# Performance work log

Hardware: AMD Instinct MI355X
Metric: run time of the kernel (lower is better)

Reference implementation:

```python
import jax, jax.numpy as jnp
import numpy as np

B, D, K, H, N = 2048, 3, 64, 768, 4096  # batch, tree depth, fanout, hidden, internal nodes


def setup_inputs() -> dict:
    key = jax.random.key(0)
    k1, k2, k3, k4, k5 = jax.random.split(key, 5)
    pooled = jax.random.normal(k1, (B, H), dtype=jnp.float32)
    nodes = jax.random.randint(k2, (B, D), 0, N)            # per-sample fc head ids along the label path
    path = jax.random.randint(k3, (B, D), 0, K)             # per-node CE target (child index)
    W = jax.random.normal(k4, (N, K, H), dtype=jnp.float32) * 0.02  # stacked nn.Linear weights
    b = jax.random.normal(k5, (N, K), dtype=jnp.float32) * 0.02     # stacked nn.Linear biases
    return {"pooled": pooled, "nodes": nodes, "path": path, "W": W, "b": b}


def reference(pooled, nodes, path, W, b):
    # Gather each sample's tiny linear heads along its label path: [B, D, K, H]
    Wg = W[nodes]
    bg = b[nodes]                                            # [B, D, K]
    # Per-sample, per-depth gemv: fc[n](feature) for n in nodes
    logits = jnp.einsum('bdkh,bh->bdk', Wg, pooled) + bg     # [B, D, K]
    # Per-node CrossEntropyLoss against path targets, summed over the path
    lse = jax.nn.logsumexp(logits, axis=-1)                  # [B, D]
    tgt = jnp.take_along_axis(logits, path[..., None], axis=-1)[..., 0]  # [B, D]
    losses = jnp.sum(lse - tgt, axis=-1)                     # [B]
    return losses, logits
```

## Files before the change

### kernel.cpp

```cpp
#include <hip/hip_runtime.h>
#include <hip/hip_bf16.h>

#define BATCH   2048
#define DEPTH   3
#define FANOUT  64
#define HID     768
#define NNODES  4096
#define NPAIRS  (BATCH * DEPTH)
#define CAP     16
#define NTAIL   64
#define SCHUNK  4

#define WS_COUNT 0
#define WS_OCNT  NNODES
#define WS_LIST  (NNODES + 4)
#define WS_OVFL  (WS_LIST + NNODES * CAP)
#define WS_ZERO_INTS (NNODES + 4)

__global__ __launch_bounds__(256) void bin_kernel(const int* __restrict__ nodes,
                                                  int* __restrict__ ws) {
    int idx = blockIdx.x * 256 + threadIdx.x;
    if (idx >= NPAIRS) return;
    int n = nodes[idx];
    int pos = atomicAdd(&ws[WS_COUNT + n], 1);
    if (pos < CAP) {
        ws[WS_LIST + n * CAP + pos] = idx;
    } else {
        int op = atomicAdd(&ws[WS_OCNT], 1);
        ws[WS_OVFL + op] = idx;
    }
}

template <int SC>
__device__ __forceinline__ void compute_rows(
    const float4* __restrict__ w4,
    const float (*s_pool)[HID],
    float (*s_log)[FANOUT],
    const float* s_bias,
    int wave, int lane)
{
#pragma unroll 4
    for (int kk = 0; kk < 16; ++kk) {
        const int k = wave * 16 + kk;
        const float4* wr = w4 + (size_t)k * (HID / 4);
        float4 w0 = wr[lane], w1 = wr[lane + 64], w2 = wr[lane + 128];
        float v[SC];
#pragma unroll
        for (int s = 0; s < SC; ++s) {
            const float4* a4 = reinterpret_cast<const float4*>(&s_pool[s][0]);
            float4 a0 = a4[lane], a1 = a4[lane + 64], a2 = a4[lane + 128];
            v[s] = w0.x * a0.x + w0.y * a0.y + w0.z * a0.z + w0.w * a0.w
                 + w1.x * a1.x + w1.y * a1.y + w1.z * a1.z + w1.w * a1.w
                 + w2.x * a2.x + w2.y * a2.y + w2.z * a2.z + w2.w * a2.w;
        }
#pragma unroll
        for (int off = 32; off > 0; off >>= 1) {
#pragma unroll
            for (int s = 0; s < SC; ++s)
                v[s] += __shfl_xor(v[s], off, 64);
        }
        if (lane == 0) {
#pragma unroll
            for (int s = 0; s < SC; ++s)
                s_log[s][k] = v[s] + s_bias[k];
        }
    }
}

__global__ __launch_bounds__(256) void node_gemm_kernel(
    const float* __restrict__ pooled,
    const float* __restrict__ W,
    const float* __restrict__ bias,
    const int*   __restrict__ nodes,
    int*         __restrict__ ws,
    float*       __restrict__ logits)
{
    __shared__ int   s_pairs[CAP];
    __shared__ float s_bias[FANOUT];
    __shared__ float s_pool[SCHUNK][HID];
    __shared__ float s_log[SCHUNK][FANOUT];

    const int tid  = threadIdx.x;
    const int wave = tid >> 6;
    const int lane = tid & 63;

    int c = 0;
    int n = -1;

    if (blockIdx.x < NNODES) {
        n = blockIdx.x;
        c = ws[WS_COUNT + n];
        if (c == 0) return;
        c = min(c, CAP);
        if (tid < c) s_pairs[tid] = ws[WS_LIST + (size_t)n * CAP + tid];
    } else {
        const int oc = min(ws[WS_OCNT], NPAIRS);
        const int i  = (int)blockIdx.x - NNODES;
        if (i >= oc) return;
        c = 1;
        if (tid == 0) s_pairs[0] = ws[WS_OVFL + i];
        __syncthreads();
        n = nodes[s_pairs[0]];
    }
    if (tid < FANOUT) s_bias[tid] = bias[(size_t)n * FANOUT + tid];
    __syncthreads();

    const float4* w4 = reinterpret_cast<const float4*>(W + (size_t)n * FANOUT * HID);

    for (int base = 0; base < c; base += SCHUNK) {
        const int sc = min(c - base, SCHUNK);
        const int* pair_chunk = s_pairs + base;

        for (int idx = tid; idx < sc * (HID / 4); idx += 256) {
            int s = idx / (HID / 4);
            int f = idx % (HID / 4);
            int b = pair_chunk[s] / DEPTH;
            reinterpret_cast<float4*>(&s_pool[s][0])[f] =
                reinterpret_cast<const float4*>(pooled + (size_t)b * HID)[f];
        }
        __syncthreads();

        switch (sc) {
        case 1: compute_rows<1>(w4, s_pool, s_log, s_bias, wave, lane); break;
        case 2: compute_rows<2>(w4, s_pool, s_log, s_bias, wave, lane); break;
        case 3: compute_rows<3>(w4, s_pool, s_log, s_bias, wave, lane); break;
        default: compute_rows<4>(w4, s_pool, s_log, s_bias, wave, lane); break;
        }
        __syncthreads();

        for (int idx = tid; idx < sc * FANOUT; idx += 256) {
            int s = idx >> 6, k = idx & 63;
            logits[(size_t)pair_chunk[s] * FANOUT + k] = s_log[s][k];
        }
        __syncthreads();
    }
}

__global__ __launch_bounds__(256) void loss_kernel(
    const float* __restrict__ logits,
    const int*   __restrict__ path,
    float*       __restrict__ losses)
{
    const int wave = threadIdx.x >> 6;
    const int lane = threadIdx.x & 63;
    const int b = blockIdx.x * 4 + wave;
    if (b >= BATCH) return;
    const float* lg = logits + (size_t)b * DEPTH * FANOUT;
    float loss = 0.f;
#pragma unroll
    for (int d = 0; d < DEPTH; ++d) {
        float x = lg[d * FANOUT + lane];
        float m = x;
#pragma unroll
        for (int off = 32; off > 0; off >>= 1)
            m = fmaxf(m, __shfl_xor(m, off, 64));
        float e = expf(x - m);
#pragma unroll
        for (int off = 32; off > 0; off >>= 1)
            e += __shfl_xor(e, off, 64);
        float lse = m + logf(e);
        int t = path[b * DEPTH + d];
        loss += lse - __shfl(x, t, 64);
    }
    if (lane == 0) losses[b] = loss;
}

extern "C" void kernel_launch(void* const* d_in, const int* in_sizes, int n_in,
                              void* d_out, int out_size, void* d_ws, size_t ws_size,
                              hipStream_t stream) {
    const float* pooled = (const float*)d_in[0];
    const int*   nodes  = (const int*)d_in[1];
    const int*   path   = (const int*)d_in[2];
    const float* W      = (const float*)d_in[3];
    const float* bias   = (const float*)d_in[4];

    float* losses = (float*)d_out;
    float* logits = (float*)d_out + BATCH;
    int*   ws     = (int*)d_ws;

    hipMemsetAsync(ws, 0, WS_ZERO_INTS * sizeof(int), stream);
    hipLaunchKernelGGL(bin_kernel, dim3((NPAIRS + 255) / 256), dim3(256),
                       0, stream, nodes, ws);
    hipLaunchKernelGGL(node_gemm_kernel, dim3(NNODES + NTAIL), dim3(256),
                       0, stream, pooled, W, bias, nodes, ws, logits);
    hipLaunchKernelGGL(loss_kernel, dim3((BATCH + 3) / 4), dim3(256),
                       0, stream, logits, path, losses);
}
```

Measured before the change: 134.9 us.

## Fuse binning, node GEMV and loss into one persistent cooperative kernel

Replaces the three launches (binning, per-node GEMV, loss) with a single cooperative persistent kernel. Blocks pull work from an atomic queue that holds only the active nodes, and each node's per-pair cross-entropy term is computed in place while the logits are still in shared memory. Grid-wide syncs separate the phases, and a final pass sums the per-depth terms. This removes launch gaps and idle blocks for unused nodes, at the cost of grid.sync overhead, contention on the atomic queue, and a fallback path if the cooperative launch fails.

```diff
diff --git a/kernel.cpp b/kernel.cpp
--- a/kernel.cpp
+++ b/kernel.cpp
@@ -1,5 +1,8 @@
 #include <hip/hip_runtime.h>
 #include <hip/hip_bf16.h>
+#include <hip/hip_cooperative_groups.h>
+
+namespace cg = cooperative_groups;
 
 #define BATCH   2048
 #define DEPTH   3
@@ -10,12 +13,187 @@
 #define CAP     16
 #define NTAIL   64
 #define SCHUNK  4
+#define NCU     256
 
 #define WS_COUNT 0
-#define WS_OCNT  NNODES
-#define WS_LIST  (NNODES + 4)
+#define WS_OCNT  4096
+#define WS_NACT  4097
+#define WS_QHEAD 4098
+#define WS_ACT   4100
+#define WS_LIST  (WS_ACT + NNODES)
 #define WS_OVFL  (WS_LIST + NNODES * CAP)
-#define WS_ZERO_INTS (NNODES + 4)
+#define WS_PART  (WS_OVFL + NPAIRS)
+#define WS_ZERO_INTS 4100
+
+template <int SC>
+__device__ __forceinline__ void compute_rows(
+    const float4* __restrict__ w4,
+    const float (*s_pool)[HID],
+    float (*s_log)[FANOUT],
+    const float* s_bias,
+    int wave, int lane)
+{
+#pragma unroll 4
+    for (int kk = 0; kk < 16; ++kk) {
+        const int k = wave * 16 + kk;
+        const float4* wr = w4 + (size_t)k * (HID / 4);
+        float4 w0 = wr[lane], w1 = wr[lane + 64], w2 = wr[lane + 128];
+        float v[SC];
+#pragma unroll
+        for (int s = 0; s < SC; ++s) {
+            const float4* a4 = reinterpret_cast<const float4*>(&s_pool[s][0]);
+            float4 a0 = a4[lane], a1 = a4[lane + 64], a2 = a4[lane + 128];
+            v[s] = w0.x * a0.x + w0.y * a0.y + w0.z * a0.z + w0.w * a0.w
+                 + w1.x * a1.x + w1.y * a1.y + w1.z * a1.z + w1.w * a1.w
+                 + w2.x * a2.x + w2.y * a2.y + w2.z * a2.z + w2.w * a2.w;
+        }
+#pragma unroll
+        for (int off = 32; off > 0; off >>= 1) {
+#pragma unroll
+            for (int s = 0; s < SC; ++s)
+                v[s] += __shfl_xor(v[s], off, 64);
+        }
+        if (lane == 0) {
+#pragma unroll
+            for (int s = 0; s < SC; ++s)
+                s_log[s][k] = v[s] + s_bias[k];
+        }
+    }
+}
+
+template <bool WITH_PART>
+__device__ __forceinline__ void process_node(
+    const float* __restrict__ pooled,
+    const float* __restrict__ W,
+    const int*   __restrict__ path,
+    float*       __restrict__ logits,
+    float*       __restrict__ part,
+    const int* s_pairs, int c, int n,
+    const float* s_bias,
+    float (*s_pool)[HID], float (*s_log)[FANOUT],
+    int tid, int wave, int lane)
+{
+    const float4* w4 = reinterpret_cast<const float4*>(W + (size_t)n * FANOUT * HID);
+    for (int base = 0; base < c; base += SCHUNK) {
+        const int sc = min(c - base, SCHUNK);
+        const int* pair_chunk = s_pairs + base;
+
+        for (int idx = tid; idx < sc * (HID / 4); idx += 256) {
+            int s = idx / (HID / 4), f = idx % (HID / 4);
+            int b = pair_chunk[s] / DEPTH;
+            reinterpret_cast<float4*>(&s_pool[s][0])[f] =
+                reinterpret_cast<const float4*>(pooled + (size_t)b * HID)[f];
+        }
+        __syncthreads();
+
+        switch (sc) {
+        case 1: compute_rows<1>(w4, s_pool, s_log, s_bias, wave, lane); break;
+        case 2: compute_rows<2>(w4, s_pool, s_log, s_bias, wave, lane); break;
+        case 3: compute_rows<3>(w4, s_pool, s_log, s_bias, wave, lane); break;
+        default: compute_rows<4>(w4, s_pool, s_log, s_bias, wave, lane); break;
+        }
+        __syncthreads();
+
+        for (int idx = tid; idx < sc * FANOUT; idx += 256) {
+            int s = idx >> 6, k = idx & 63;
+            logits[(size_t)pair_chunk[s] * FANOUT + k] = s_log[s][k];
+        }
+        if (WITH_PART) {
+            for (int s = wave; s < sc; s += 4) {
+                int pair = pair_chunk[s];
+                float x = s_log[s][lane];
+                float m = x;
+#pragma unroll
+                for (int off = 32; off > 0; off >>= 1)
+                    m = fmaxf(m, __shfl_xor(m, off, 64));
+                float e = expf(x - m);
+#pragma unroll
+                for (int off = 32; off > 0; off >>= 1)
+                    e += __shfl_xor(e, off, 64);
+                if (lane == 0) {
+                    int t = path[pair];
+                    part[pair] = m + logf(e) - s_log[s][t];
+                }
+            }
+        }
+        __syncthreads();
+    }
+}
+
+__global__ __launch_bounds__(256) void fused_kernel(
+    const float* __restrict__ pooled,
+    const float* __restrict__ W,
+    const float* __restrict__ bias,
+    const int*   __restrict__ nodes,
+    const int*   __restrict__ path,
+    int*         __restrict__ ws,
+    float*       __restrict__ losses,
+    float*       __restrict__ logits)
+{
+    cg::grid_group grid = cg::this_grid();
+    const int tid  = threadIdx.x;
+    const int wave = tid >> 6;
+    const int lane = tid & 63;
+    const int gstride = gridDim.x * 256;
+    float* part = reinterpret_cast<float*>(ws) + WS_PART;
+
+    for (int idx = blockIdx.x * 256 + tid; idx < NPAIRS; idx += gstride) {
+        int n = nodes[idx];
+        int pos = atomicAdd(&ws[WS_COUNT + n], 1);
+        if (pos == 0) {
+            int a = atomicAdd(&ws[WS_NACT], 1);
+            ws[WS_ACT + a] = n;
+        }
+        if (pos < CAP) {
+            ws[WS_LIST + n * CAP + pos] = idx;
+        } else {
+            int op = atomicAdd(&ws[WS_OCNT], 1);
+            ws[WS_OVFL + op] = idx;
+        }
+    }
+    __threadfence();
+    grid.sync();
+
+    __shared__ int   s_i;
+    __shared__ int   s_pairs[CAP];
+    __shared__ float s_bias[FANOUT];
+    __shared__ float s_pool[SCHUNK][HID];
+    __shared__ float s_log[SCHUNK][FANOUT];
+
+    const int nact = ws[WS_NACT];
+    const int oc   = min(ws[WS_OCNT], NPAIRS);
+    const int ntot = nact + oc;
+
+    for (;;) {
+        if (tid == 0) s_i = atomicAdd(&ws[WS_QHEAD], 1);
+        __syncthreads();
+        const int i = s_i;
+        if (i >= ntot) break;
+
+        int n, c;
+        if (i < nact) {
+            n = ws[WS_ACT + i];
+            c = min(ws[WS_COUNT + n], CAP);
+            if (tid < c) s_pairs[tid] = ws[WS_LIST + n * CAP + tid];
+        } else {
+            int pair = ws[WS_OVFL + (i - nact)];
+            n = nodes[pair];
+            c = 1;
+            if (tid == 0) s_pairs[0] = pair;
+        }
+        if (tid < FANOUT) s_bias[tid] = bias[(size_t)n * FANOUT + tid];
+        __syncthreads();
+
+        process_node<true>(pooled, W, path, logits, part,
+                           s_pairs, c, n, s_bias, s_pool, s_log, tid, wave, lane);
+    }
+
+    __threadfence();
+    grid.sync();
+
+    for (int b = blockIdx.x * 256 + tid; b < BATCH; b += gstride)
+        losses[b] = part[b * 3 + 0] + part[b * 3 + 1] + part[b * 3 + 2];
+}
 
 __global__ __launch_bounds__(256) void bin_kernel(const int* __restrict__ nodes,
                                                   int* __restrict__ ws) {
@@ -31,42 +209,6 @@
     }
 }
 
-template <int SC>
-__device__ __forceinline__ void compute_rows(
-    const float4* __restrict__ w4,
-    const float (*s_pool)[HID],
-    float (*s_log)[FANOUT],
-    const float* s_bias,
-    int wave, int lane)
-{
-#pragma unroll 4
-    for (int kk = 0; kk < 16; ++kk) {
-        const int k = wave * 16 + kk;
-        const float4* wr = w4 + (size_t)k * (HID / 4);
-        float4 w0 = wr[lane], w1 = wr[lane + 64], w2 = wr[lane + 128];
-        float v[SC];
-#pragma unroll
-        for (int s = 0; s < SC; ++s) {
-            const float4* a4 = reinterpret_cast<const float4*>(&s_pool[s][0]);
-            float4 a0 = a4[lane], a1 = a4[lane + 64], a2 = a4[lane + 128];
-            v[s] = w0.x * a0.x + w0.y * a0.y + w0.z * a0.z + w0.w * a0.w
-                 + w1.x * a1.x + w1.y * a1.y + w1.z * a1.z + w1.w * a1.w
-                 + w2.x * a2.x + w2.y * a2.y + w2.z * a2.z + w2.w * a2.w;
-        }
-#pragma unroll
-        for (int off = 32; off > 0; off >>= 1) {
-#pragma unroll
-            for (int s = 0; s < SC; ++s)
-                v[s] += __shfl_xor(v[s], off, 64);
-        }
-        if (lane == 0) {
-#pragma unroll
-            for (int s = 0; s < SC; ++s)
-                s_log[s][k] = v[s] + s_bias[k];
-        }
-    }
-}
-
 __global__ __launch_bounds__(256) void node_gemm_kernel(
     const float* __restrict__ pooled,
     const float* __restrict__ W,
@@ -84,9 +226,7 @@
     const int wave = tid >> 6;
     const int lane = tid & 63;
 
-    int c = 0;
-    int n = -1;
-
+    int c = 0, n = -1;
     if (blockIdx.x < NNODES) {
         n = blockIdx.x;
         c = ws[WS_COUNT + n];
@@ -94,9 +234,9 @@
         c = min(c, CAP);
         if (tid < c) s_pairs[tid] = ws[WS_LIST + (size_t)n * CAP + tid];
     } else {
-        const int oc = min(ws[WS_OCNT], NPAIRS);
+        const int ocnt = min(ws[WS_OCNT], NPAIRS);
         const int i  = (int)blockIdx.x - NNODES;
-        if (i >= oc) return;
+        if (i >= ocnt) return;
         c = 1;
         if (tid == 0) s_pairs[0] = ws[WS_OVFL + i];
         __syncthreads();
@@ -105,35 +245,8 @@
     if (tid < FANOUT) s_bias[tid] = bias[(size_t)n * FANOUT + tid];
     __syncthreads();
 
-    const float4* w4 = reinterpret_cast<const float4*>(W + (size_t)n * FANOUT * HID);
-
-    for (int base = 0; base < c; base += SCHUNK) {
-        const int sc = min(c - base, SCHUNK);
-        const int* pair_chunk = s_pairs + base;
-
-        for (int idx = tid; idx < sc * (HID / 4); idx += 256) {
-            int s = idx / (HID / 4);
-            int f = idx % (HID / 4);
-            int b = pair_chunk[s] / DEPTH;
-            reinterpret_cast<float4*>(&s_pool[s][0])[f] =
-                reinterpret_cast<const float4*>(pooled + (size_t)b * HID)[f];
-        }
-        __syncthreads();
-
-        switch (sc) {
-        case 1: compute_rows<1>(w4, s_pool, s_log, s_bias, wave, lane); break;
-        case 2: compute_rows<2>(w4, s_pool, s_log, s_bias, wave, lane); break;
-        case 3: compute_rows<3>(w4, s_pool, s_log, s_bias, wave, lane); break;
-        default: compute_rows<4>(w4, s_pool, s_log, s_bias, wave, lane); break;
-        }
-        __syncthreads();
-
-        for (int idx = tid; idx < sc * FANOUT; idx += 256) {
-            int s = idx >> 6, k = idx & 63;
-            logits[(size_t)pair_chunk[s] * FANOUT + k] = s_log[s][k];
-        }
-        __syncthreads();
-    }
+    process_node<false>(pooled, W, nullptr, logits, nullptr,
+                        s_pairs, c, n, s_bias, s_pool, s_log, tid, wave, lane);
 }
 
 __global__ __launch_bounds__(256) void loss_kernel(
@@ -179,10 +292,25 @@
     int*   ws     = (int*)d_ws;
 
     hipMemsetAsync(ws, 0, WS_ZERO_INTS * sizeof(int), stream);
-    hipLaunchKernelGGL(bin_kernel, dim3((NPAIRS + 255) / 256), dim3(256),
-                       0, stream, nodes, ws);
-    hipLaunchKernelGGL(node_gemm_kernel, dim3(NNODES + NTAIL), dim3(256),
-                       0, stream, pooled, W, bias, nodes, ws, logits);
-    hipLaunchKernelGGL(loss_kernel, dim3((BATCH + 3) / 4), dim3(256),
-                       0, stream, logits, path, losses);
-}
+
+    int nb = 0;
+    hipError_t qerr = hipOccupancyMaxActiveBlocksPerMultiprocessor(
+        &nb, (const void*)fused_kernel, 256, 0);
+    if (qerr != hipSuccess || nb < 1) nb = 1;
+    if (nb > 8) nb = 8;
+    dim3 grid(nb * NCU), block(256);
+
+    void* args[] = {(void*)&pooled, (void*)&W, (void*)&bias, (void*)&nodes,
+                    (void*)&path, (void*)&ws, (void*)&losses, (void*)&logits};
+    hipError_t lerr = hipLaunchCooperativeKernel(
+        (const void*)fused_kernel, grid, block, args, 0, stream);
+
+    if (lerr != hipSuccess) {
+        hipLaunchKernelGGL(bin_kernel, dim3((NPAIRS + 255) / 256), dim3(256),
+                           0, stream, nodes, ws);
+        hipLaunchKernelGGL(node_gemm_kernel, dim3(NNODES + NTAIL), dim3(256),
+                           0, stream, pooled, W, bias, nodes, ws, logits);
+        hipLaunchKernelGGL(loss_kernel, dim3((BATCH + 3) / 4), dim3(256),
+                           0, stream, logits, path, losses);
+    }
+}
```

After: 375.1 us. 2.78x slower.

## Fuse per-pair cross-entropy into node GEMM and remap node block order

Applied to the files above, without the earlier changes.

Each node block now computes the logsumexp-minus-target partial loss for its pairs from shared-memory logits and writes it to workspace. A tiny kernel then sums the three depth partials per sample, replacing the loss kernel that re-read all logits from global memory. The node-to-block mapping is also permuted (interleaved by 8) to spread adjacent nodes across XCDs or channels. This adds per-wave reductions inside the GEMM kernel and a workspace dependency.

```diff
diff --git a/kernel.cpp b/kernel.cpp
--- a/kernel.cpp
+++ b/kernel.cpp
@@ -15,6 +15,7 @@
 #define WS_OCNT  NNODES
 #define WS_LIST  (NNODES + 4)
 #define WS_OVFL  (WS_LIST + NNODES * CAP)
+#define WS_PART  (WS_OVFL + NPAIRS)
 #define WS_ZERO_INTS (NNODES + 4)
 
 __global__ __launch_bounds__(256) void bin_kernel(const int* __restrict__ nodes,
@@ -72,6 +73,7 @@
     const float* __restrict__ W,
     const float* __restrict__ bias,
     const int*   __restrict__ nodes,
+    const int*   __restrict__ path,
     int*         __restrict__ ws,
     float*       __restrict__ logits)
 {
@@ -83,12 +85,14 @@
     const int tid  = threadIdx.x;
     const int wave = tid >> 6;
     const int lane = tid & 63;
+    float* part = reinterpret_cast<float*>(ws) + WS_PART;
 
     int c = 0;
     int n = -1;
 
     if (blockIdx.x < NNODES) {
-        n = blockIdx.x;
+        const int orig = blockIdx.x;
+        n = (orig & 7) * (NNODES / 8) + (orig >> 3);
         c = ws[WS_COUNT + n];
         if (c == 0) return;
         c = min(c, CAP);
@@ -132,37 +136,33 @@
             int s = idx >> 6, k = idx & 63;
             logits[(size_t)pair_chunk[s] * FANOUT + k] = s_log[s][k];
         }
+
+        for (int s = wave; s < sc; s += 4) {
+            int pair = pair_chunk[s];
+            float x = s_log[s][lane];
+            float m = x;
+#pragma unroll
+            for (int off = 32; off > 0; off >>= 1)
+                m = fmaxf(m, __shfl_xor(m, off, 64));
+            float e = expf(x - m);
+#pragma unroll
+            for (int off = 32; off > 0; off >>= 1)
+                e += __shfl_xor(e, off, 64);
+            if (lane == 0) {
+                int t = path[pair];
+                part[pair] = m + logf(e) - s_log[s][t];
+            }
+        }
         __syncthreads();
     }
 }
 
-__global__ __launch_bounds__(256) void loss_kernel(
-    const float* __restrict__ logits,
-    const int*   __restrict__ path,
-    float*       __restrict__ losses)
-{
-    const int wave = threadIdx.x >> 6;
-    const int lane = threadIdx.x & 63;
-    const int b = blockIdx.x * 4 + wave;
-    if (b >= BATCH) return;
-    const float* lg = logits + (size_t)b * DEPTH * FANOUT;
-    float loss = 0.f;
-#pragma unroll
-    for (int d = 0; d < DEPTH; ++d) {
-        float x = lg[d * FANOUT + lane];
-        float m = x;
-#pragma unroll
-        for (int off = 32; off > 0; off >>= 1)
-            m = fmaxf(m, __shfl_xor(m, off, 64));
-        float e = expf(x - m);
-#pragma unroll
-        for (int off = 32; off > 0; off >>= 1)
-            e += __shfl_xor(e, off, 64);
-        float lse = m + logf(e);
-        int t = path[b * DEPTH + d];
-        loss += lse - __shfl(x, t, 64);
-    }
-    if (lane == 0) losses[b] = loss;
+__global__ __launch_bounds__(256) void loss_sum_kernel(const int* __restrict__ ws,
+                                                       float* __restrict__ losses) {
+    const float* part = reinterpret_cast<const float*>(ws) + WS_PART;
+    int b = blockIdx.x * 256 + threadIdx.x;
+    if (b < BATCH)
+        losses[b] = part[b * 3 + 0] + part[b * 3 + 1] + part[b * 3 + 2];
 }
 
 extern "C" void kernel_launch(void* const* d_in, const int* in_sizes, int n_in,
@@ -182,7 +182,7 @@
     hipLaunchKernelGGL(bin_kernel, dim3((NPAIRS + 255) / 256), dim3(256),
                        0, stream, nodes, ws);
     hipLaunchKernelGGL(node_gemm_kernel, dim3(NNODES + NTAIL), dim3(256),
-                       0, stream, pooled, W, bias, nodes, ws, logits);
-    hipLaunchKernelGGL(loss_kernel, dim3((BATCH + 3) / 4), dim3(256),
-                       0, stream, logits, path, losses);
+                       0, stream, pooled, W, bias, nodes, path, ws, logits);
+    hipLaunchKernelGGL(loss_sum_kernel, dim3((BATCH + 255) / 256), dim3(256),
+                       0, stream, ws, losses);
 }
```

Measured after the change: 136.7 us. About the same (+1.4%).
